# Kernel optimization log

Measured on AMD Instinct MI355X. Metric: run time of the kernel, lower is better.

The kernel has to match this reference:

```python
import jax, jax.numpy as jnp
import numpy as np

B, L, D, H, FF = 4, 1024, 768, 12, 3072
DK = D // H
P = 32          # num_postags
MAXD = 256      # max relative distance


def _ln(x, g, b, eps):
    mu = jnp.mean(x, axis=-1, keepdims=True)
    var = jnp.mean(jnp.square(x - mu), axis=-1, keepdims=True)
    return (x - mu) * jax.lax.rsqrt(var + eps) * g + b


def setup_inputs() -> dict:
    key = jax.random.key(0)
    ks = jax.random.split(key, 16)
    s = 0.02
    return {
        "x": jax.random.normal(ks[0], (B, L, D), jnp.float32),
        "postag_ids": jax.random.randint(ks[1], (B, L), 0, P),
        "lex_mask": jax.random.normal(ks[2], (B, L), jnp.float32),
        "ln1_g": jnp.ones((D,), jnp.float32),
        "ln1_b": jnp.zeros((D,), jnp.float32),
        "Wq": jax.random.normal(ks[3], (D, D), jnp.float32) * s,
        "bq": jnp.zeros((D,), jnp.float32),
        "Wk": jax.random.normal(ks[4], (D, D), jnp.float32) * s,
        "bk": jnp.zeros((D,), jnp.float32),
        "Wv": jax.random.normal(ks[5], (D, D), jnp.float32) * s,
        "bv": jnp.zeros((D,), jnp.float32),
        "Wo": jax.random.normal(ks[6], (D, D), jnp.float32) * s,
        "bo": jnp.zeros((D,), jnp.float32),
        "rel_emb": jax.random.normal(ks[7], (2 * MAXD + 1, H), jnp.float32) * s,
        "postag_table": jax.random.normal(ks[8], (P * P, H), jnp.float32) * s,
        "ln2_g": jnp.ones((D,), jnp.float32),
        "ln2_b": jnp.zeros((D,), jnp.float32),
        "W1": jax.random.normal(ks[9], (D, FF), jnp.float32) * s,
        "b1": jnp.zeros((FF,), jnp.float32),
        "W2": jax.random.normal(ks[10], (FF, D), jnp.float32) * s,
        "b2": jnp.zeros((D,), jnp.float32),
    }


def reference(x, postag_ids, lex_mask, ln1_g, ln1_b, Wq, bq, Wk, bk, Wv, bv,
              Wo, bo, rel_emb, postag_table, ln2_g, ln2_b, W1, b1, W2, b2):
    # ---- pre-LN self-attention with rel-pos + postag + lex additive biases ----
    q_in = _ln(x, ln1_g, ln1_b, 1e-6)
    Q = (q_in @ Wq + bq).reshape(B, L, H, DK).transpose(0, 2, 1, 3)  # [B,H,L,dk]
    K = (q_in @ Wk + bk).reshape(B, L, H, DK).transpose(0, 2, 1, 3)
    V = (q_in @ Wv + bv).reshape(B, L, H, DK).transpose(0, 2, 1, 3)

    logits = jnp.einsum("bhld,bhsd->bhls", Q, K) / jnp.sqrt(jnp.float32(DK))

    # relative position bias: [H, L, L]
    idx = jnp.arange(L)
    rel = idx[None, :] - idx[:, None]
    clipped = jnp.clip(rel, -MAXD, MAXD) + MAXD
    pos_bias = rel_emb[clipped].transpose(2, 0, 1)  # [H,L,L]

    # postag pair bias: [B, H, L, L]
    pair = postag_ids[:, :, None] * P + postag_ids[:, None, :]  # [B,L,L]
    pt_bias = postag_table[pair].transpose(0, 3, 1, 2)  # [B,H,L,L]

    logits = logits + pos_bias[None] + pt_bias + lex_mask[:, None, None, :]

    attn = jax.nn.softmax(logits, axis=-1)
    out = jnp.einsum("bhls,bhsd->bhld", attn, V)
    out = out.transpose(0, 2, 1, 3).reshape(B, L, D)
    out = out @ Wo + bo + x  # residual

    # ---- FeedForward (pre-LN, exact GELU) ----
    h = _ln(out, ln2_g, ln2_b, 1e-5)
    h = jax.nn.gelu(h @ W1 + b1, approximate=False)
    return out + h @ W2 + b2
```

## Files before the change

### kernel.cpp

```cpp
#include <hip/hip_runtime.h>
#include <hip/hip_bf16.h>
#include <math.h>

typedef __hip_bfloat16 bf16;
typedef __attribute__((ext_vector_type(8))) short short8;
typedef __attribute__((ext_vector_type(4))) float f32x4;

#define BB 4
#define LL 1024
#define DD 768
#define HH 12
#define DK 64
#define FF_ 3072
#define PP 32
#define MAXD 256

__device__ __forceinline__ void async_load16(const void* g, void* l) {
    __builtin_amdgcn_global_load_lds(
        (const __attribute__((address_space(1))) unsigned int*)g,
        (__attribute__((address_space(3))) unsigned int*)l, 16, 0, 0);
}

__global__ __launch_bounds__(256) void ln_kernel(const float* __restrict__ x,
                                                 const float* __restrict__ g,
                                                 const float* __restrict__ b,
                                                 float eps,
                                                 bf16* __restrict__ y) {
    const int row = blockIdx.x;
    const int tid = threadIdx.x;
    const float* xr = x + (size_t)row * DD;

    float v[3];
    float s = 0.f, ss = 0.f;
#pragma unroll
    for (int i = 0; i < 3; ++i) {
        float t = xr[tid + i * 256];
        v[i] = t; s += t; ss += t * t;
    }
    __shared__ float rs[256], rss[256];
    rs[tid] = s; rss[tid] = ss;
    __syncthreads();
    for (int off = 128; off; off >>= 1) {
        if (tid < off) { rs[tid] += rs[tid + off]; rss[tid] += rss[tid + off]; }
        __syncthreads();
    }
    const float mean = rs[0] * (1.f / DD);
    const float var  = rss[0] * (1.f / DD) - mean * mean;
    const float inv  = rsqrtf(var + eps);
#pragma unroll
    for (int i = 0; i < 3; ++i) {
        int c = tid + i * 256;
        y[(size_t)row * DD + c] = __float2bfloat16((v[i] - mean) * inv * g[c] + b[c]);
    }
}

__global__ __launch_bounds__(256) void prep_ln(
        const float* __restrict__ x,
        const float* __restrict__ ln1_g, const float* __restrict__ ln1_b,
        const float* __restrict__ Wq, const float* __restrict__ Wk,
        const float* __restrict__ Wv, const float* __restrict__ Wo,
        const float* __restrict__ W1, const float* __restrict__ W2,
        const float* __restrict__ bq, const float* __restrict__ bk,
        const float* __restrict__ bv,
        bf16* __restrict__ y_ln,
        bf16* __restrict__ WtQKV, bf16* __restrict__ WtO,
        bf16* __restrict__ Wt1, bf16* __restrict__ Wt2,
        float* __restrict__ bqkv) {
    const int bid = blockIdx.x;
    const int tid = threadIdx.x;

    if (bid < 4096) {
        const float* xr = x + (size_t)bid * DD;
        float v[3];
        float s = 0.f, ss = 0.f;
#pragma unroll
        for (int i = 0; i < 3; ++i) {
            float t = xr[tid + i * 256];
            v[i] = t; s += t; ss += t * t;
        }
        __shared__ float rs[256], rss[256];
        rs[tid] = s; rss[tid] = ss;
        __syncthreads();
        for (int off = 128; off; off >>= 1) {
            if (tid < off) { rs[tid] += rs[tid + off]; rss[tid] += rss[tid + off]; }
            __syncthreads();
        }
        const float mean = rs[0] * (1.f / DD);
        const float var  = rss[0] * (1.f / DD) - mean * mean;
        const float inv  = rsqrtf(var + 1e-6f);
#pragma unroll
        for (int i = 0; i < 3; ++i) {
            int c = tid + i * 256;
            y_ln[(size_t)bid * DD + c] = __float2bfloat16((v[i] - mean) * inv * ln1_g[c] + ln1_b[c]);
        }
        return;
    }
    if (bid >= 11008) {
        int i = (bid - 11008) * 256 + tid;
        if (i < 2304) {
            float v = (i < 768) ? bq[i] : (i < 1536) ? bk[i - 768] : bv[i - 1536];
            bqkv[i] = v;
        }
        return;
    }
    const int tb = bid - 4096;
    const float* W; bf16* Wt; int K, N, tile;
    if (tb < 576)       { W = Wq; Wt = WtQKV;                      K = DD;  N = DD;  tile = tb; }
    else if (tb < 1152) { W = Wk; Wt = WtQKV + (size_t)768 * DD;   K = DD;  N = DD;  tile = tb - 576; }
    else if (tb < 1728) { W = Wv; Wt = WtQKV + (size_t)1536 * DD;  K = DD;  N = DD;  tile = tb - 1152; }
    else if (tb < 2304) { W = Wo; Wt = WtO;                        K = DD;  N = DD;  tile = tb - 1728; }
    else if (tb < 4608) { W = W1; Wt = Wt1;                        K = DD;  N = FF_; tile = tb - 2304; }
    else                { W = W2; Wt = Wt2;                        K = FF_; N = DD;  tile = tb - 4608; }
    const int ntn = N / 32;
    const int n0 = (tile % ntn) * 32, k0 = (tile / ntn) * 32;

    __shared__ float tilebuf[32][33];
    const int tx = tid & 31, ty = tid >> 5;
#pragma unroll
    for (int i = 0; i < 4; ++i) {
        int k = ty + i * 8;
        tilebuf[k][tx] = W[(size_t)(k0 + k) * N + n0 + tx];
    }
    __syncthreads();
#pragma unroll
    for (int i = 0; i < 4; ++i) {
        int n = ty + i * 8;
        Wt[(size_t)(n0 + n) * K + k0 + tx] = __float2bfloat16(tilebuf[tx][n]);
    }
}

__global__ __launch_bounds__(256) void ff2_reduce(const bf16* __restrict__ Fp,
                                                  const float* __restrict__ out1,
                                                  const float* __restrict__ b2,
                                                  float* __restrict__ dout) {
    const size_t stride = (size_t)BB * LL * DD;
    const size_t i8 = ((size_t)blockIdx.x * 256 + threadIdx.x) * 8;
    const int c = (int)(i8 % DD);

    float acc[8];
    float4 r0 = *(const float4*)(out1 + i8);
    float4 r1 = *(const float4*)(out1 + i8 + 4);
    float4 bb0 = *(const float4*)(b2 + c);
    float4 bb1 = *(const float4*)(b2 + c + 4);
    acc[0] = r0.x + bb0.x; acc[1] = r0.y + bb0.y; acc[2] = r0.z + bb0.z; acc[3] = r0.w + bb0.w;
    acc[4] = r1.x + bb1.x; acc[5] = r1.y + bb1.y; acc[6] = r1.z + bb1.z; acc[7] = r1.w + bb1.w;
#pragma unroll
    for (int p = 0; p < 4; ++p) {
        short8 v = *(const short8*)(Fp + p * stride + i8);
#pragma unroll
        for (int k = 0; k < 8; ++k) acc[k] += __bfloat162float(((const bf16*)&v)[k]);
    }
    float4 o0 = {acc[0], acc[1], acc[2], acc[3]};
    float4 o1 = {acc[4], acc[5], acc[6], acc[7]};
    *(float4*)(dout + i8) = o0;
    *(float4*)(dout + i8 + 4) = o1;
}

template <int TM, int TN, int RES, bool GELU, bool SPLIT_QKV, int KSPLIT, typename OutT>
__global__ __launch_bounds__(256) void mfma_gemm_bt(const bf16* __restrict__ A,
                                                    const bf16* __restrict__ Bt,
                                                    const float* __restrict__ bias,
                                                    const float* __restrict__ res,
                                                    OutT* __restrict__ C,
                                                    bf16* __restrict__ QhOut,
                                                    bf16* __restrict__ KhOut,
                                                    bf16* __restrict__ VtOut,
                                                    int M, int N, int K) {
    constexpr int WM = TM / 32;
    constexpr int WN = TN / 32;
    constexpr int CA = TM / 64;
    constexpr int CB = TN / 64;
    __shared__ short As[2][TM * 32];
    __shared__ short Bs[2][TN * 32];

    const int L = blockIdx.x + gridDim.x * (blockIdx.y + gridDim.y * blockIdx.z);
    const int xcd = L & 7, j = L >> 3;
    const int col = j % gridDim.x;
    const int panel = xcd + 8 * (j / gridDim.x);
    const int byy = panel % gridDim.y;
    const int bzz = panel / gridDim.y;

    const int bm = byy * TM, bn = col * TN;
    const int tid = threadIdx.x;
    const int w = tid >> 6, lane = tid & 63;
    const int c16 = lane & 15, quad = lane >> 4;
    const int wy = w >> 1, wx = w & 1;

    const int srow_in = lane >> 2;
    const int cg = (lane & 3) ^ quad;

    const int Ksub = K / KSPLIT;
    const int kbase = bzz * Ksub;

    f32x4 acc[WM][WN];
#pragma unroll
    for (int i = 0; i < WM; ++i)
#pragma unroll
        for (int j2 = 0; j2 < WN; ++j2) acc[i][j2] = (f32x4)0.f;

    auto stage = [&](int buf, int k0) {
#pragma unroll
        for (int j2 = 0; j2 < CA; ++j2) {
            const int ci = w * CA + j2;
            const int row = ci * 16 + srow_in;
            async_load16(A + (size_t)(bm + row) * K + k0 + cg * 8, (char*)As[buf] + ci * 1024);
        }
#pragma unroll
        for (int j2 = 0; j2 < CB; ++j2) {
            const int ci = w * CB + j2;
            const int row = ci * 16 + srow_in;
            async_load16(Bt + (size_t)(bn + row) * K + k0 + cg * 8, (char*)Bs[buf] + ci * 1024);
        }
    };

    const int nIter = Ksub / 32;
    stage(0, kbase);
    for (int kt = 0; kt < nIter; ++kt) {
        const int buf = kt & 1;
        __syncthreads();
        if (kt + 1 < nIter) stage(buf ^ 1, kbase + (kt + 1) * 32);

        short8 af[WM], bf[WN];
#pragma unroll
        for (int i = 0; i < WM; ++i) {
            const int ra = wy * (WM * 16) + i * 16 + c16;
            const int ca = quad ^ ((ra >> 2) & 3);
            af[i] = *(const short8*)((const char*)As[buf] + ra * 64 + ca * 16);
        }
#pragma unroll
        for (int i = 0; i < WN; ++i) {
            const int rb = wx * (WN * 16) + i * 16 + c16;
            const int cb = quad ^ ((rb >> 2) & 3);
            bf[i] = *(const short8*)((const char*)Bs[buf] + rb * 64 + cb * 16);
        }
#pragma unroll
        for (int mi = 0; mi < WM; ++mi)
#pragma unroll
            for (int ni = 0; ni < WN; ++ni)
                acc[mi][ni] = __builtin_amdgcn_mfma_f32_16x16x32_bf16(af[mi], bf[ni], acc[mi][ni], 0, 0, 0);
    }

    if (KSPLIT > 1) {
        OutT* Cp = C + (size_t)bzz * M * N;
#pragma unroll
        for (int mi = 0; mi < WM; ++mi)
#pragma unroll
            for (int ni = 0; ni < WN; ++ni) {
                const int n = bn + wx * (WN * 16) + ni * 16 + c16;
#pragma unroll
                for (int r = 0; r < 4; ++r) {
                    const int m = bm + wy * (WM * 16) + mi * 16 + quad * 4 + r;
                    if constexpr (sizeof(OutT) == 2)
                        Cp[(size_t)m * N + n] = __float2bfloat16(acc[mi][ni][r]);
                    else
                        Cp[(size_t)m * N + n] = acc[mi][ni][r];
                }
            }
        return;
    }

    if (SPLIT_QKV) {
        bf16* dst; int base;
        if (bn < 768)       { dst = QhOut; base = 0; }
        else if (bn < 1536) { dst = KhOut; base = 768; }
        else                { dst = VtOut; base = 1536; }
#pragma unroll
        for (int mi = 0; mi < WM; ++mi) {
#pragma unroll
            for (int ni = 0; ni < WN; ++ni) {
                const int nfull = bn + wx * (WN * 16) + ni * 16 + c16;
                const float bv = bias[nfull];
                const int nr = nfull - base;
                const int hv = nr >> 6, dv = nr & 63;
#pragma unroll
                for (int r = 0; r < 4; ++r) {
                    const int m = bm + wy * (WM * 16) + mi * 16 + quad * 4 + r;
                    const float v = acc[mi][ni][r] + bv;
                    const size_t bh = (size_t)((m >> 10) * HH + hv);
                    if (base == 1536)
                        dst[(bh * DK + dv) * LL + (m & 1023)] = __float2bfloat16(v);
                    else
                        dst[(bh * LL + (m & 1023)) * DK + dv] = __float2bfloat16(v);
                }
            }
        }
        return;
    }

#pragma unroll
    for (int mi = 0; mi < WM; ++mi) {
#pragma unroll
        for (int ni = 0; ni < WN; ++ni) {
            const int n = bn + wx * (WN * 16) + ni * 16 + c16;
            const float bv = bias[n];
#pragma unroll
            for (int r = 0; r < 4; ++r) {
                const int m = bm + wy * (WM * 16) + mi * 16 + quad * 4 + r;
                float v = acc[mi][ni][r] + bv;
                if (GELU) v = 0.5f * v * (1.f + erff(v * 0.70710678118f));
                if (RES == 2) v += res[(size_t)m * N + n];
                if constexpr (sizeof(OutT) == 2)
                    C[(size_t)m * N + n] = __float2bfloat16(v);
                else
                    C[(size_t)m * N + n] = v;
            }
        }
    }
}

__global__ __launch_bounds__(256) void flash_attn_kernel(
        const bf16* __restrict__ Qh, const bf16* __restrict__ Kh, const bf16* __restrict__ Vt,
        const int* __restrict__ postag, const float* __restrict__ lex,
        const float* __restrict__ rel_emb, const float* __restrict__ pt_table,
        bf16* __restrict__ O) {
    const int qt = blockIdx.x;
    const int h  = blockIdx.y;
    const int b  = blockIdx.z;
    const int tid  = threadIdx.x;
    const int w    = tid >> 6;
    const int lane = tid & 63;
    const int c    = lane & 15;
    const int quad = lane >> 4;

    __shared__ short Ks[4096];
    __shared__ short Vs[4096];
    __shared__ bf16  Ps[4][16][72];
    __shared__ f32x4 relT[516];
    __shared__ float pt_col[1024];
    __shared__ float lex_f[LL];
    __shared__ short ps_f[LL];

    for (int i = tid; i < 516; i += 256) {
        f32x4 t;
        t[0] = rel_emb[min(i, 512) * HH + h];
        t[1] = rel_emb[min(max(i - 1, 0), 512) * HH + h];
        t[2] = rel_emb[min(max(i - 2, 0), 512) * HH + h];
        t[3] = rel_emb[min(max(i - 3, 0), 512) * HH + h];
        relT[i] = t;
    }
    for (int i = tid; i < 1024; i += 256) {
        pt_col[i] = pt_table[i * HH + h];
        lex_f[i]  = lex[b * LL + i];
        ps_f[i]   = (short)postag[b * LL + i];
    }

    const int q0 = qt * 64 + w * 16;
    const size_t bh = (size_t)(b * HH + h);
    const bf16* Kbase = Kh + bh * LL * DK;
    const bf16* Vbase = Vt + bh * DK * LL;

    short8 qf0, qf1;
    {
        const bf16* qp = Qh + (bh * LL + q0 + c) * DK + quad * 8;
        qf0 = *(const short8*)qp;
        qf1 = *(const short8*)(qp + 32);
    }
    int plx_r[4];
#pragma unroll
    for (int r = 0; r < 4; ++r) plx_r[r] = postag[b * LL + q0 + quad * 4 + r] * PP;

    f32x4 o_acc[4];
#pragma unroll
    for (int t = 0; t < 4; ++t) o_acc[t] = (f32x4)0.f;
    float lsum[4] = {0.f, 0.f, 0.f, 0.f};

    const int srow = lane >> 3;
    const int schunk = lane & 7;
    __syncthreads();

    for (int s0 = 0; s0 < LL; s0 += 64) {
#pragma unroll
        for (int j = 0; j < 2; ++j) {
            const int row = w * 16 + j * 8 + srow;
            const int g = schunk ^ (row & 7);
            async_load16(Kbase + (size_t)(s0 + row) * DK + g * 8,
                         (char*)Ks + (w * 16 + j * 8) * 128);
            async_load16(Vbase + (size_t)row * LL + s0 + g * 8,
                         (char*)Vs + (w * 16 + j * 8) * 128);
        }
        __syncthreads();

        f32x4 S[4];
#pragma unroll
        for (int t = 0; t < 4; ++t) {
            const int r = t * 16 + c;
            short8 kf0 = *(const short8*)&Ks[r * 64 + ((quad ^ (r & 7)) * 8)];
            short8 kf1 = *(const short8*)&Ks[r * 64 + (((4 + quad) ^ (r & 7)) * 8)];
            f32x4 a = (f32x4)0.f;
            a = __builtin_amdgcn_mfma_f32_16x16x32_bf16(qf0, kf0, a, 0, 0, 0);
            a = __builtin_amdgcn_mfma_f32_16x16x32_bf16(qf1, kf1, a, 0, 0, 0);
            S[t] = a;
        }

        const int d0 = s0 - q0;
        if (d0 >= 271 || d0 <= -319) {
            const float rcv = (d0 >= 271) ? relT[515][0] : relT[0][0];
#pragma unroll
            for (int t = 0; t < 4; ++t) {
                const int s_glob = s0 + t * 16 + c;
                const float lx = lex_f[s_glob] + rcv;
                const int   ps = ps_f[s_glob];
#pragma unroll
                for (int r = 0; r < 4; ++r) {
                    float e = __expf(S[t][r] * 0.125f + pt_col[plx_r[r] + ps] + lx);
                    S[t][r] = e;
                    lsum[r] += e;
                }
            }
        } else {
            const int ebase = d0 - quad * 4 + 256;
#pragma unroll
            for (int t = 0; t < 4; ++t) {
                const int s_loc = t * 16 + c;
                const int s_glob = s0 + s_loc;
                const float lx = lex_f[s_glob];
                const int   ps = ps_f[s_glob];
                const int e = min(max(ebase + s_loc, 0), 515);
                f32x4 rv = relT[e];
#pragma unroll
                for (int r = 0; r < 4; ++r) {
                    float ev = __expf(S[t][r] * 0.125f + rv[r] + pt_col[plx_r[r] + ps] + lx);
                    S[t][r] = ev;
                    lsum[r] += ev;
                }
            }
        }

#pragma unroll
        for (int t = 0; t < 4; ++t)
#pragma unroll
            for (int r = 0; r < 4; ++r)
                Ps[w][quad * 4 + r][t * 16 + c] = __float2bfloat16(S[t][r]);

        short8 pa0 = *(const short8*)&Ps[w][c][quad * 8];
        short8 pa1 = *(const short8*)&Ps[w][c][quad * 8 + 32];

#pragma unroll
        for (int t = 0; t < 4; ++t) {
            const int r = t * 16 + c;
            short8 vf0 = *(const short8*)&Vs[r * 64 + ((quad ^ (r & 7)) * 8)];
            short8 vf1 = *(const short8*)&Vs[r * 64 + (((4 + quad) ^ (r & 7)) * 8)];
            o_acc[t] = __builtin_amdgcn_mfma_f32_16x16x32_bf16(pa0, vf0, o_acc[t], 0, 0, 0);
            o_acc[t] = __builtin_amdgcn_mfma_f32_16x16x32_bf16(pa1, vf1, o_acc[t], 0, 0, 0);
        }
        __syncthreads();
    }

#pragma unroll
    for (int mm = 1; mm < 16; mm <<= 1)
#pragma unroll
        for (int r = 0; r < 4; ++r) lsum[r] += __shfl_xor(lsum[r], mm);

    float inv_l[4];
#pragma unroll
    for (int r = 0; r < 4; ++r) inv_l[r] = 1.f / lsum[r];
#pragma unroll
    for (int t = 0; t < 4; ++t)
#pragma unroll
        for (int r = 0; r < 4; ++r) {
            const int row = q0 + quad * 4 + r;
            O[((size_t)(b * LL + row)) * DD + h * DK + t * 16 + c] =
                __float2bfloat16(o_acc[t][r] * inv_l[r]);
        }
}

extern "C" void kernel_launch(void* const* d_in, const int* in_sizes, int n_in,
                              void* d_out, int out_size, void* d_ws, size_t ws_size,
                              hipStream_t stream) {
    const float* x          = (const float*)d_in[0];
    const int*   postag_ids = (const int*)d_in[1];
    const float* lex_mask   = (const float*)d_in[2];
    const float* ln1_g      = (const float*)d_in[3];
    const float* ln1_b      = (const float*)d_in[4];
    const float* Wq         = (const float*)d_in[5];
    const float* bq         = (const float*)d_in[6];
    const float* Wk         = (const float*)d_in[7];
    const float* bk         = (const float*)d_in[8];
    const float* Wv         = (const float*)d_in[9];
    const float* bv         = (const float*)d_in[10];
    const float* Wo         = (const float*)d_in[11];
    const float* bo         = (const float*)d_in[12];
    const float* rel_emb    = (const float*)d_in[13];
    const float* pt_table   = (const float*)d_in[14];
    const float* ln2_g      = (const float*)d_in[15];
    const float* ln2_b      = (const float*)d_in[16];
    const float* W1         = (const float*)d_in[17];
    const float* b1         = (const float*)d_in[18];
    const float* W2         = (const float*)d_in[19];
    const float* b2         = (const float*)d_in[20];

    const int M = BB * LL;
    char* ws = (char*)d_ws;
    size_t off = 0;
    bf16* y_ln  = (bf16*)(ws + off); off += (size_t)M * DD * 2;
    bf16* Qh    = (bf16*)(ws + off); off += (size_t)M * DD * 2;
    bf16* Kh    = (bf16*)(ws + off); off += (size_t)M * DD * 2;
    bf16* Vt    = (bf16*)(ws + off); off += (size_t)M * DD * 2;
    bf16* attn  = (bf16*)(ws + off); off += (size_t)M * DD * 2;
    bf16* h2    = (bf16*)(ws + off); off += (size_t)M * DD * 2;
    float* out1 = (float*)(ws + off); off += (size_t)M * DD * 4;
    bf16* ff1   = (bf16*)(ws + off); off += (size_t)M * FF_ * 2;
    bf16* WtQKV = (bf16*)(ws + off); off += (size_t)2304 * DD * 2;
    bf16* WtO   = (bf16*)(ws + off); off += (size_t)DD * DD * 2;
    bf16* Wt1   = (bf16*)(ws + off); off += (size_t)FF_ * DD * 2;
    bf16* Wt2   = (bf16*)(ws + off); off += (size_t)DD * FF_ * 2;
    float* bqkv = (float*)(ws + off); off += (size_t)2304 * 4;
    bf16*  PartF2 = (bf16*)ws;

    prep_ln<<<11017, 256, 0, stream>>>(x, ln1_g, ln1_b, Wq, Wk, Wv, Wo, W1, W2,
                                       bq, bk, bv, y_ln, WtQKV, WtO, Wt1, Wt2, bqkv);

    mfma_gemm_bt<64, 128, 0, false, true, 1, bf16><<<dim3(2304 / 128, M / 64), 256, 0, stream>>>(
        y_ln, WtQKV, bqkv, nullptr, (bf16*)nullptr, Qh, Kh, Vt, M, 2304, DD);

    flash_attn_kernel<<<dim3(LL / 64, HH, BB), 256, 0, stream>>>(
        Qh, Kh, Vt, postag_ids, lex_mask, rel_emb, pt_table, attn);

    mfma_gemm_bt<64, 64, 2, false, false, 1, float><<<dim3(DD / 64, M / 64), 256, 0, stream>>>(
        attn, WtO, bo, x, out1, nullptr, nullptr, nullptr, M, DD, DD);

    ln_kernel<<<M, 256, 0, stream>>>(out1, ln2_g, ln2_b, 1e-5f, h2);

    mfma_gemm_bt<128, 128, 0, true, false, 1, bf16><<<dim3(FF_ / 128, M / 128), 256, 0, stream>>>(
        h2, Wt1, b1, nullptr, ff1, nullptr, nullptr, nullptr, M, FF_, DD);

    mfma_gemm_bt<128, 128, 0, false, false, 4, bf16><<<dim3(DD / 128, M / 128, 4), 256, 0, stream>>>(
        ff1, Wt2, nullptr, nullptr, PartF2, nullptr, nullptr, nullptr, M, DD, FF_);

    ff2_reduce<<<(M * DD / 8) / 256, 256, 0, stream>>>(PartF2, out1, b2, (float*)d_out);
}
```

Before: 291.5 us.

## Load K/V fragments straight into registers with next-tile prefetch, dropping LDS staging

The attention kernel no longer stages K and V tiles through shared memory with async loads and per-tile barriers. Each wave now reads its MFMA operand fragments directly from global memory into registers, and loads the next tile's fragments while the current tile is being computed. This removes the LDS round-trip and the two block-wide syncs per iteration. In exchange, every wave in a block fetches the same K/V data (four times the global/L2 traffic), and register pressure rises noticeably. The prefetch on the final iteration also reads past the end of the head's K/V slice.

```diff
diff --git a/kernel.cpp b/kernel.cpp
--- a/kernel.cpp
+++ b/kernel.cpp
@@ -322,8 +322,6 @@
     const int c    = lane & 15;
     const int quad = lane >> 4;
 
-    __shared__ short Ks[4096];
-    __shared__ short Vs[4096];
     __shared__ bf16  Ps[4][16][72];
     __shared__ f32x4 relT[516];
     __shared__ float pt_col[1024];
@@ -364,32 +362,36 @@
     for (int t = 0; t < 4; ++t) o_acc[t] = (f32x4)0.f;
     float lsum[4] = {0.f, 0.f, 0.f, 0.f};
 
-    const int srow = lane >> 3;
-    const int schunk = lane & 7;
+    short8 kf0[4], kf1[4], vf0[4], vf1[4];
+#pragma unroll
+    for (int t = 0; t < 4; ++t) {
+        const bf16* kp = Kbase + (size_t)(t * 16 + c) * DK + quad * 8;
+        kf0[t] = *(const short8*)kp;
+        kf1[t] = *(const short8*)(kp + 32);
+        const bf16* vp = Vbase + (size_t)(t * 16 + c) * LL + quad * 8;
+        vf0[t] = *(const short8*)vp;
+        vf1[t] = *(const short8*)(vp + 32);
+    }
+
     __syncthreads();
 
-    for (int s0 = 0; s0 < LL; s0 += 64) {
-#pragma unroll
-        for (int j = 0; j < 2; ++j) {
-            const int row = w * 16 + j * 8 + srow;
-            const int g = schunk ^ (row & 7);
-            async_load16(Kbase + (size_t)(s0 + row) * DK + g * 8,
-                         (char*)Ks + (w * 16 + j * 8) * 128);
-            async_load16(Vbase + (size_t)row * LL + s0 + g * 8,
-                         (char*)Vs + (w * 16 + j * 8) * 128);
-        }
-        __syncthreads();
+    for (int tt = 0; tt < LL / 64; ++tt) {
+        const int s0 = tt * 64;
 
         f32x4 S[4];
 #pragma unroll
         for (int t = 0; t < 4; ++t) {
-            const int r = t * 16 + c;
-            short8 kf0 = *(const short8*)&Ks[r * 64 + ((quad ^ (r & 7)) * 8)];
-            short8 kf1 = *(const short8*)&Ks[r * 64 + (((4 + quad) ^ (r & 7)) * 8)];
             f32x4 a = (f32x4)0.f;
-            a = __builtin_amdgcn_mfma_f32_16x16x32_bf16(qf0, kf0, a, 0, 0, 0);
-            a = __builtin_amdgcn_mfma_f32_16x16x32_bf16(qf1, kf1, a, 0, 0, 0);
+            a = __builtin_amdgcn_mfma_f32_16x16x32_bf16(qf0, kf0[t], a, 0, 0, 0);
+            a = __builtin_amdgcn_mfma_f32_16x16x32_bf16(qf1, kf1[t], a, 0, 0, 0);
             S[t] = a;
+        }
+
+#pragma unroll
+        for (int t = 0; t < 4; ++t) {
+            const bf16* kp = Kbase + (size_t)(s0 + 64 + t * 16 + c) * DK + quad * 8;
+            kf0[t] = *(const short8*)kp;
+            kf1[t] = *(const short8*)(kp + 32);
         }
 
         const int d0 = s0 - q0;
@@ -437,13 +439,16 @@
 
 #pragma unroll
         for (int t = 0; t < 4; ++t) {
-            const int r = t * 16 + c;
-            short8 vf0 = *(const short8*)&Vs[r * 64 + ((quad ^ (r & 7)) * 8)];
-            short8 vf1 = *(const short8*)&Vs[r * 64 + (((4 + quad) ^ (r & 7)) * 8)];
-            o_acc[t] = __builtin_amdgcn_mfma_f32_16x16x32_bf16(pa0, vf0, o_acc[t], 0, 0, 0);
-            o_acc[t] = __builtin_amdgcn_mfma_f32_16x16x32_bf16(pa1, vf1, o_acc[t], 0, 0, 0);
-        }
-        __syncthreads();
+            o_acc[t] = __builtin_amdgcn_mfma_f32_16x16x32_bf16(pa0, vf0[t], o_acc[t], 0, 0, 0);
+            o_acc[t] = __builtin_amdgcn_mfma_f32_16x16x32_bf16(pa1, vf1[t], o_acc[t], 0, 0, 0);
+        }
+
+#pragma unroll
+        for (int t = 0; t < 4; ++t) {
+            const bf16* vp = Vbase + (size_t)(t * 16 + c) * LL + s0 + 64 + quad * 8;
+            vf0[t] = *(const short8*)vp;
+            vf1[t] = *(const short8*)(vp + 32);
+        }
     }
 
 #pragma unroll
```

Measured after the change: 348.9 us. 19.7% more time.
